# Optimization experiments

Hardware: AMD Instinct MI355X
Metric: run time of the kernel (lower is better)

Reference implementation:

```python
import jax, jax.numpy as jnp
import numpy as np

NUM_EXPERTS = 8

def setup_inputs() -> dict:
    key = jax.random.key(0)
    x = jax.random.normal(key, (8192, NUM_EXPERTS, 1024), dtype=jnp.float32)
    return {"x": x}

def reference(x):
    # Gram-Schmidt orthonormalization of the num_experts vectors per batch row.
    # x: [B, E, D] -> basis: [B, E, D] with orthonormal rows along E.
    b0 = x[:, 0, :]
    b0 = b0 / jnp.linalg.norm(b0, axis=-1, keepdims=True)
    basis = b0[:, None, :]  # [B, 1, D]
    num_experts = x.shape[1]
    for i in range(1, num_experts):
        v = x[:, i, :]  # [B, D]
        # coefficients of v on current orthonormal basis: [B, k]
        coeff = jnp.einsum('bd,bkd->bk', v, basis)
        w = v - jnp.einsum('bk,bkd->bd', coeff, basis)
        wn = w / jnp.linalg.norm(w, axis=-1, keepdims=True)
        basis = jnp.concatenate([basis, wn[:, None, :]], axis=1)
    return basis
```

## Files before the change

kernel.cpp:

```cpp
#include <hip/hip_runtime.h>


constexpr int NE      = 8;
constexpr int DIM     = 1024;
constexpr int THREADS = 256;
constexpr int VPT     = DIM / THREADS;
constexpr int NWAVES  = THREADS / 64;

__global__ __launch_bounds__(THREADS) void gs_kernel(const float* __restrict__ x,
                                                     float* __restrict__ out) {
    const int b    = blockIdx.x;
    const int tid  = threadIdx.x;
    const int lane = tid & 63;
    const int wid  = tid >> 6;
    const size_t base = (size_t)b * NE * DIM;

    float v[NE][VPT];
    #pragma unroll
    for (int e = 0; e < NE; ++e) {
        const float4 t = *reinterpret_cast<const float4*>(x + base + (size_t)e * DIM + tid * VPT);
        v[e][0] = t.x; v[e][1] = t.y; v[e][2] = t.z; v[e][3] = t.w;
    }

    __shared__ float red[NWAVES][NE];

    {
        float s = v[0][0]*v[0][0] + v[0][1]*v[0][1] + v[0][2]*v[0][2] + v[0][3]*v[0][3];
        #pragma unroll
        for (int o = 32; o > 0; o >>= 1) s += __shfl_xor(s, o);
        if (lane == 0) red[wid][0] = s;
        __syncthreads();
        const float tot = red[0][0] + red[1][0] + red[2][0] + red[3][0];
        const float inv = 1.0f / sqrtf(tot);
        #pragma unroll
        for (int j = 0; j < VPT; ++j) v[0][j] *= inv;
        __syncthreads();
        float4 t; t.x = v[0][0]; t.y = v[0][1]; t.z = v[0][2]; t.w = v[0][3];
        *reinterpret_cast<float4*>(out + base + tid * VPT) = t;
    }

    #pragma unroll
    for (int i = 1; i < NE; ++i) {
        #pragma unroll
        for (int k = 0; k < i; ++k) {
            float s = 0.0f;
            #pragma unroll
            for (int j = 0; j < VPT; ++j) s += v[i][j] * v[k][j];
            #pragma unroll
            for (int o = 32; o > 0; o >>= 1) s += __shfl_xor(s, o);
            if (lane == 0) red[wid][k] = s;
        }
        __syncthreads();
        float c[NE];
        #pragma unroll
        for (int k = 0; k < i; ++k)
            c[k] = red[0][k] + red[1][k] + red[2][k] + red[3][k];
        __syncthreads();

        #pragma unroll
        for (int k = 0; k < i; ++k) {
            #pragma unroll
            for (int j = 0; j < VPT; ++j) v[i][j] = fmaf(-c[k], v[k][j], v[i][j]);
        }

        float s = 0.0f;
        #pragma unroll
        for (int j = 0; j < VPT; ++j) s += v[i][j] * v[i][j];
        #pragma unroll
        for (int o = 32; o > 0; o >>= 1) s += __shfl_xor(s, o);
        if (lane == 0) red[wid][0] = s;
        __syncthreads();
        const float inv = 1.0f / sqrtf(red[0][0] + red[1][0] + red[2][0] + red[3][0]);
        #pragma unroll
        for (int j = 0; j < VPT; ++j) v[i][j] *= inv;
        __syncthreads();

        float4 t; t.x = v[i][0]; t.y = v[i][1]; t.z = v[i][2]; t.w = v[i][3];
        *reinterpret_cast<float4*>(out + base + (size_t)i * DIM + tid * VPT) = t;
    }
}

extern "C" void kernel_launch(void* const* d_in, const int* in_sizes, int n_in,
                              void* d_out, int out_size, void* d_ws, size_t ws_size,
                              hipStream_t stream) {
    const float* x = (const float*)d_in[0];
    float* out = (float*)d_out;
    const int batches = in_sizes[0] / (NE * DIM);
    gs_kernel<<<batches, THREADS, 0, stream>>>(x, out);
}
```

Baseline: 445.7 us.

## Replace sequential Gram-Schmidt with Gram-matrix Cholesky in a single reduction pass

Computes all 36 pairwise dot products of the 8 input vectors at once, reduces them in one shuffle pass plus one shared-memory exchange, then runs a per-thread Cholesky factorization of the Gram matrix and applies forward substitution to form the orthonormal rows. This removes about 30 block-wide barriers and the serial chain of dependent reductions of the original, leaving a single synchronisation. It also sets a min-blocks-per-CU hint in launch bounds. The trade-off is Cholesky of the Gram matrix, which is numerically less stable than classical Gram-Schmidt for ill-conditioned inputs, and higher register pressure from the 36 partial sums and L entries.

```diff
diff --git a/kernel.cpp b/kernel.cpp
--- a/kernel.cpp
+++ b/kernel.cpp
@@ -6,9 +6,10 @@
 constexpr int THREADS = 256;
 constexpr int VPT     = DIM / THREADS;
 constexpr int NWAVES  = THREADS / 64;
+constexpr int NPAIR   = NE * (NE + 1) / 2;
 
-__global__ __launch_bounds__(THREADS) void gs_kernel(const float* __restrict__ x,
-                                                     float* __restrict__ out) {
+__global__ __launch_bounds__(THREADS, 4) void gs_chol_kernel(const float* __restrict__ x,
+                                                             float* __restrict__ out) {
     const int b    = blockIdx.x;
     const int tid  = threadIdx.x;
     const int lane = tid & 63;
@@ -22,59 +23,66 @@
         v[e][0] = t.x; v[e][1] = t.y; v[e][2] = t.z; v[e][3] = t.w;
     }
 
-    __shared__ float red[NWAVES][NE];
-
-    {
-        float s = v[0][0]*v[0][0] + v[0][1]*v[0][1] + v[0][2]*v[0][2] + v[0][3]*v[0][3];
+    float p[NPAIR];
+    #pragma unroll
+    for (int i = 0; i < NE; ++i) {
         #pragma unroll
-        for (int o = 32; o > 0; o >>= 1) s += __shfl_xor(s, o);
-        if (lane == 0) red[wid][0] = s;
-        __syncthreads();
-        const float tot = red[0][0] + red[1][0] + red[2][0] + red[3][0];
-        const float inv = 1.0f / sqrtf(tot);
-        #pragma unroll
-        for (int j = 0; j < VPT; ++j) v[0][j] *= inv;
-        __syncthreads();
-        float4 t; t.x = v[0][0]; t.y = v[0][1]; t.z = v[0][2]; t.w = v[0][3];
-        *reinterpret_cast<float4*>(out + base + tid * VPT) = t;
+        for (int k = 0; k <= i; ++k) {
+            const int d = i * (i + 1) / 2 + k;
+            float s = v[i][0] * v[k][0];
+            #pragma unroll
+            for (int j = 1; j < VPT; ++j) s = fmaf(v[i][j], v[k][j], s);
+            p[d] = s;
+        }
     }
 
     #pragma unroll
-    for (int i = 1; i < NE; ++i) {
-        #pragma unroll
-        for (int k = 0; k < i; ++k) {
-            float s = 0.0f;
-            #pragma unroll
-            for (int j = 0; j < VPT; ++j) s += v[i][j] * v[k][j];
-            #pragma unroll
-            for (int o = 32; o > 0; o >>= 1) s += __shfl_xor(s, o);
-            if (lane == 0) red[wid][k] = s;
-        }
-        __syncthreads();
-        float c[NE];
-        #pragma unroll
-        for (int k = 0; k < i; ++k)
-            c[k] = red[0][k] + red[1][k] + red[2][k] + red[3][k];
-        __syncthreads();
-
-        #pragma unroll
-        for (int k = 0; k < i; ++k) {
-            #pragma unroll
-            for (int j = 0; j < VPT; ++j) v[i][j] = fmaf(-c[k], v[k][j], v[i][j]);
-        }
-
-        float s = 0.0f;
-        #pragma unroll
-        for (int j = 0; j < VPT; ++j) s += v[i][j] * v[i][j];
+    for (int d = 0; d < NPAIR; ++d) {
+        float s = p[d];
         #pragma unroll
         for (int o = 32; o > 0; o >>= 1) s += __shfl_xor(s, o);
-        if (lane == 0) red[wid][0] = s;
-        __syncthreads();
-        const float inv = 1.0f / sqrtf(red[0][0] + red[1][0] + red[2][0] + red[3][0]);
+        p[d] = s;
+    }
+
+    __shared__ alignas(16) float part[NPAIR][NWAVES];
+    if (lane == 0) {
         #pragma unroll
-        for (int j = 0; j < VPT; ++j) v[i][j] *= inv;
-        __syncthreads();
+        for (int d = 0; d < NPAIR; ++d) part[d][wid] = p[d];
+    }
+    __syncthreads();
 
+    float L[NPAIR];
+    float rinv[NE];
+    #pragma unroll
+    for (int i = 0; i < NE; ++i) {
+        #pragma unroll
+        for (int k = 0; k <= i; ++k) {
+            const int d = i * (i + 1) / 2 + k;
+            const float4 g4 = *reinterpret_cast<const float4*>(&part[d][0]);
+            float s = (g4.x + g4.y) + (g4.z + g4.w);
+            #pragma unroll
+            for (int m = 0; m < k; ++m)
+                s = fmaf(-L[i * (i + 1) / 2 + m], L[k * (k + 1) / 2 + m], s);
+            if (k == i) {
+                const float li = sqrtf(s);
+                L[d]    = li;
+                rinv[i] = 1.0f / li;
+            } else {
+                L[d] = s * rinv[k];
+            }
+        }
+    }
+
+    #pragma unroll
+    for (int i = 0; i < NE; ++i) {
+        #pragma unroll
+        for (int j = 0; j < VPT; ++j) {
+            float w = v[i][j];
+            #pragma unroll
+            for (int k = 0; k < i; ++k)
+                w = fmaf(-L[i * (i + 1) / 2 + k], v[k][j], w);
+            v[i][j] = w * rinv[i];
+        }
         float4 t; t.x = v[i][0]; t.y = v[i][1]; t.z = v[i][2]; t.w = v[i][3];
         *reinterpret_cast<float4*>(out + base + (size_t)i * DIM + tid * VPT) = t;
     }
@@ -86,5 +94,5 @@
     const float* x = (const float*)d_in[0];
     float* out = (float*)d_out;
     const int batches = in_sizes[0] / (NE * DIM);
-    gs_kernel<<<batches, THREADS, 0, stream>>>(x, out);
+    gs_chol_kernel<<<batches, THREADS, 0, stream>>>(x, out);
 }
```

New measurement: 437.2 us. About the same (-1.9%).
